# Performance work log

Measured on AMD Instinct MI355X. Metric: run time of the kernel, lower is better.

The kernel has to match this reference:

```python
import jax, jax.numpy as jnp
import numpy as np

EMB = 300
HID = 500
NUM_CLASSES = 20
WORD_VOCAB = 100000
ENT_VOCAB = 50
SEQ = 4096


def setup_inputs() -> dict:
    key = jax.random.key(0)
    ks = jax.random.split(key, 10)
    s = 0.05
    return {
        "ner_words": jax.random.randint(ks[0], (SEQ,), 0, WORD_VOCAB),
        "ner_labels": jax.random.randint(ks[1], (SEQ,), 0, ENT_VOCAB),
        "emb_word": jax.random.normal(ks[2], (WORD_VOCAB, EMB), jnp.float32) * s,
        "emb_ent": jax.random.normal(ks[3], (ENT_VOCAB, EMB), jnp.float32) * s,
        "W_ih": jax.random.normal(ks[4], (4 * HID, 2 * EMB), jnp.float32) * s,
        "W_hh": jax.random.normal(ks[5], (4 * HID, HID), jnp.float32) * s,
        "b_ih": jax.random.normal(ks[6], (4 * HID,), jnp.float32) * s,
        "b_hh": jax.random.normal(ks[7], (4 * HID,), jnp.float32) * s,
        "fc_w": jax.random.normal(ks[8], (NUM_CLASSES, HID), jnp.float32) * s,
        "fc_b": jax.random.normal(ks[9], (NUM_CLASSES,), jnp.float32) * s,
    }


def _lstm_last(x, W_ih, W_hh, b_ih, b_hh):
    # x: [N, 2*EMB]. PyTorch LSTM gate order: i, f, g, o.
    pre = x @ W_ih.T + (b_ih + b_hh)  # [N, 4H] input contribution precomputed

    def step(carry, p):
        h, c = carry
        gates = p + h @ W_hh.T  # [4H]
        i, f, g, o = jnp.split(gates, 4)
        i = jax.nn.sigmoid(i)
        f = jax.nn.sigmoid(f)
        g = jnp.tanh(g)
        o = jax.nn.sigmoid(o)
        c = f * c + i * g
        h = o * jnp.tanh(c)
        return (h, c), None

    h0 = jnp.zeros((HID,), x.dtype)
    c0 = jnp.zeros((HID,), x.dtype)
    (h, _), _ = jax.lax.scan(step, (h0, c0), pre)
    return h  # last hidden state == last LSTM output


def reference(ner_words, ner_labels, emb_word, emb_ent, W_ih, W_hh, b_ih, b_hh, fc_w, fc_b):
    # per-token embedding gather + concat -> [N, 600]
    x = jnp.concatenate([emb_word[ner_words], emb_ent[ner_labels]], axis=-1)
    h_last = _lstm_last(x, W_ih, W_hh, b_ih, b_hh)
    out = h_last @ fc_w.T + fc_b
    return out.reshape(1, -1)
```

## Files before the change

### kernel.cpp

```cpp
#include <hip/hip_runtime.h>

typedef unsigned int uint;
typedef unsigned long long u64;
typedef _Float16 f16x2 __attribute__((ext_vector_type(2)));

#define SEQ 4096
#define EMB 300
#define HID 500
#define NG 2000
#define KX 600
#define KXP 608

#define BM 64
#define BN 64
#define BK 16

#define NWG 25
#define UPW 20
#define TPB 640

#define HPAIR 8
#define HHALF (250 * HPAIR)
#define HTOT  (2 * HHALF)

__global__ __launch_bounds__(256) void gather_x(const int* __restrict__ words,
                                                const int* __restrict__ labels,
                                                const float* __restrict__ embw,
                                                const float* __restrict__ embe,
                                                float* __restrict__ x) {
  int t = blockIdx.x;
  int w = words[t], l = labels[t];
  const float* rw = embw + (size_t)w * EMB;
  const float* re = embe + (size_t)l * EMB;
  float* xr = x + (size_t)t * KXP;
  for (int k = threadIdx.x; k < KXP; k += 256) {
    float v = 0.f;
    if (k < EMB) v = rw[k];
    else if (k < KX) v = re[k - EMB];
    xr[k] = v;
  }
}

__global__ __launch_bounds__(256) void gemm_pre(const float* __restrict__ x,
                                                const float* __restrict__ Wih,
                                                const float* __restrict__ bih,
                                                const float* __restrict__ bhh,
                                                float* __restrict__ pre) {
  __shared__ float As[BK][BM + 4];
  __shared__ float Bs[BK][BN + 4];
  const int m0 = blockIdx.x * BM;
  const int n0 = blockIdx.y * BN;
  const int tid = threadIdx.x;
  const int tx = tid & 15, ty = tid >> 4;
  const int lrow = tid >> 2;
  const int lc4 = (tid & 3) << 2;
  float acc[4][4] = {};

  for (int kk = 0; kk < KX; kk += BK) {
    float4 av = *(const float4*)(x + (size_t)(m0 + lrow) * KXP + kk + lc4);
    int brow = n0 + lrow; if (brow >= NG) brow = 0;
    float4 bv;
    if (kk + lc4 + 3 < KX) {
      bv = *(const float4*)(Wih + (size_t)brow * KX + kk + lc4);
    } else {
      float tmp[4];
#pragma unroll
      for (int j = 0; j < 4; ++j) {
        int k = kk + lc4 + j;
        tmp[j] = (k < KX) ? Wih[(size_t)brow * KX + k] : 0.f;
      }
      bv = make_float4(tmp[0], tmp[1], tmp[2], tmp[3]);
    }
    As[lc4 + 0][lrow] = av.x; As[lc4 + 1][lrow] = av.y;
    As[lc4 + 2][lrow] = av.z; As[lc4 + 3][lrow] = av.w;
    Bs[lc4 + 0][lrow] = bv.x; Bs[lc4 + 1][lrow] = bv.y;
    Bs[lc4 + 2][lrow] = bv.z; Bs[lc4 + 3][lrow] = bv.w;
    __syncthreads();
#pragma unroll
    for (int k = 0; k < BK; ++k) {
      float4 a = *(const float4*)&As[k][ty << 2];
      float4 b = *(const float4*)&Bs[k][tx << 2];
      acc[0][0] += a.x * b.x; acc[0][1] += a.x * b.y; acc[0][2] += a.x * b.z; acc[0][3] += a.x * b.w;
      acc[1][0] += a.y * b.x; acc[1][1] += a.y * b.y; acc[1][2] += a.y * b.z; acc[1][3] += a.y * b.w;
      acc[2][0] += a.z * b.x; acc[2][1] += a.z * b.y; acc[2][2] += a.z * b.z; acc[2][3] += a.z * b.w;
      acc[3][0] += a.w * b.x; acc[3][1] += a.w * b.y; acc[3][2] += a.w * b.z; acc[3][3] += a.w * b.w;
    }
    __syncthreads();
  }
#pragma unroll
  for (int i = 0; i < 4; ++i) {
    int m = m0 + (ty << 2) + i;
#pragma unroll
    for (int j = 0; j < 4; ++j) {
      int n = n0 + (tx << 2) + j;
      if (n < NG) pre[(size_t)m * NG + n] = acc[i][j] + bih[n] + bhh[n];
    }
  }
}

__global__ void init_sync(u64* hbuf) {
  for (int i = threadIdx.x; i < HTOT; i += 1024) hbuf[i] = 0ull;
}

__device__ __forceinline__ float sigm(float x) { return 1.f / (1.f + __expf(-x)); }
__device__ __forceinline__ float fast_tanh(float x) {
  x = fminf(fmaxf(x, -15.f), 15.f);
  float e = __expf(2.f * x);
  return (e - 1.f) / (e + 1.f);
}
__device__ __forceinline__ f16x2 as_f16x2(uint u) {
  union { uint i; f16x2 h; } c; c.i = u; return c.h;
}
__device__ __forceinline__ uint f2h16(float f) {
  union { _Float16 h; unsigned short u; } c; c.h = (_Float16)f; return (uint)c.u;
}
#if __has_builtin(__builtin_amdgcn_fdot2)
__device__ __forceinline__ float FDOT2(f16x2 a, f16x2 b, float c) {
  return __builtin_amdgcn_fdot2(a, b, c, false);
}
#else
__device__ __forceinline__ float FDOT2(f16x2 a, f16x2 b, float c) {
  return c + (float)a.x * (float)b.x + (float)a.y * (float)b.y;
}
#endif

#define TAGMASK 0x0000FFFF0000FFFFull

__global__ __launch_bounds__(TPB) void lstm_seq(const float* __restrict__ pre,
                                                const float* __restrict__ Whh,
                                                const float* __restrict__ fcw,
                                                const float* __restrict__ fcb,
                                                uint* hbuf,
                                                float* __restrict__ out) {
  __shared__ uint h2b[2][256];
  const int g = blockIdx.x;
  const int tid = threadIdx.x;
  const int unit = tid >> 5;
  const int gi = (tid >> 3) & 3;
  const int cc = tid & 7;
  const int owner = ((tid & 31) == 0);
  const int base = tid & 32;
  const int my_prerow = gi * HID + g * UPW + unit;
  const int my_unit = g * UPW + unit;
  const int my_slot = (my_unit >> 1) * (2 * HPAIR) + (my_unit & 1);

  for (int i = tid; i < 512; i += TPB) ((uint*)h2b)[i] = 0u;

  uint wreg[32];
  {
    size_t grow = (size_t)(gi * HID + g * UPW + unit) * HID;
#pragma unroll
    for (int q = 0; q < 8; ++q) {
#pragma unroll
      for (int j = 0; j < 4; ++j) {
        int word = q * 32 + cc * 4 + j;
        int c2 = word * 2;
        float v0 = (c2 < HID) ? Whh[grow + c2] : 0.f;
        float v1 = (c2 + 1 < HID) ? Whh[grow + c2 + 1] : 0.f;
        wreg[q * 4 + j] = f2h16(v0) | (f2h16(v1) << 16);
      }
    }
  }

  const u64* hb64 = (const u64*)hbuf;
  float c_reg = 0.f;

  for (int t = 0; t < SEQ; ++t) {
    float pre_v = 0.f;
    if (cc == 0) pre_v = pre[(size_t)t * NG + my_prerow];

    const u64 want2 = (u64)((uint)t & 0xffffu) * 0x0000000100000001ull;
    if (tid < 250) {
      const u64* src = hb64 + (size_t)(t & 1) * HHALF + (size_t)tid * HPAIR;
      u64 a = __hip_atomic_load(src, __ATOMIC_RELAXED, __HIP_MEMORY_SCOPE_AGENT);
      u64 b = __hip_atomic_load(src, __ATOMIC_RELAXED, __HIP_MEMORY_SCOPE_AGENT);
      for (;;) {
        if ((a & TAGMASK) == want2) break;
        if ((b & TAGMASK) == want2) { a = b; break; }
        a = __hip_atomic_load(src, __ATOMIC_RELAXED, __HIP_MEMORY_SCOPE_AGENT);
        b = __hip_atomic_load(src, __ATOMIC_RELAXED, __HIP_MEMORY_SCOPE_AGENT);
      }
      h2b[t & 1][tid] = (((uint)(a >> 16)) & 0xffffu) | (((uint)(a >> 48)) << 16);
    }
    __syncthreads();

    const uint* h2 = h2b[t & 1];
    float acc = 0.f;
#pragma unroll
    for (int q = 0; q < 8; ++q) {
      uint4 hh = *(const uint4*)&h2[q * 32 + cc * 4];
      acc = FDOT2(as_f16x2(wreg[q * 4 + 0]), as_f16x2(hh.x), acc);
      acc = FDOT2(as_f16x2(wreg[q * 4 + 1]), as_f16x2(hh.y), acc);
      acc = FDOT2(as_f16x2(wreg[q * 4 + 2]), as_f16x2(hh.z), acc);
      acc = FDOT2(as_f16x2(wreg[q * 4 + 3]), as_f16x2(hh.w), acc);
    }
    acc += __shfl_xor(acc, 1);
    acc += __shfl_xor(acc, 2);
    acc += __shfl_xor(acc, 4);
    if (cc == 0) acc += pre_v;

    float si = __shfl(acc, base + 0);
    float sf = __shfl(acc, base + 8);
    float sg = __shfl(acc, base + 16);
    float so = __shfl(acc, base + 24);
    if (owner) {
      float iv = sigm(si);
      float fv = sigm(sf);
      float gv = fast_tanh(sg);
      float ov = sigm(so);
      c_reg = fv * c_reg + iv * gv;
      float h = ov * fast_tanh(c_reg);
      uint pk = (f2h16(h) << 16) | ((uint)(t + 1) & 0xffffu);
      __hip_atomic_store(&hbuf[((t + 1) & 1) * (2 * HHALF) + my_slot], pk,
                         __ATOMIC_RELAXED, __HIP_MEMORY_SCOPE_AGENT);
    }
  }

  if (g == 0) {
    const u64 want2 = (u64)((uint)SEQ & 0xffffu) * 0x0000000100000001ull;
    if (tid < 250) {
      const u64* src = hb64 + (size_t)tid * HPAIR;
      u64 a;
      do {
        a = __hip_atomic_load(src, __ATOMIC_RELAXED, __HIP_MEMORY_SCOPE_AGENT);
      } while ((a & TAGMASK) != want2);
      h2b[0][tid] = (((uint)(a >> 16)) & 0xffffu) | (((uint)(a >> 48)) << 16);
    }
    __syncthreads();
    int row = tid >> 5, ln = tid & 31;
    float s = 0.f;
    for (int j = ln; j < HID; j += 32) {
      f16x2 p = as_f16x2(h2b[0][j >> 1]);
      float hv = (j & 1) ? (float)p.y : (float)p.x;
      s += fcw[row * HID + j] * hv;
    }
    s += __shfl_xor(s, 1); s += __shfl_xor(s, 2);
    s += __shfl_xor(s, 4); s += __shfl_xor(s, 8);
    s += __shfl_xor(s, 16);
    if (ln == 0) out[row] = s + fcb[row];
  }
}

extern "C" void kernel_launch(void* const* d_in, const int* in_sizes, int n_in,
                              void* d_out, int out_size, void* d_ws, size_t ws_size,
                              hipStream_t stream) {
  const int* words = (const int*)d_in[0];
  const int* labels = (const int*)d_in[1];
  const float* embw = (const float*)d_in[2];
  const float* embe = (const float*)d_in[3];
  const float* Wih = (const float*)d_in[4];
  const float* Whh = (const float*)d_in[5];
  const float* bih = (const float*)d_in[6];
  const float* bhh = (const float*)d_in[7];
  const float* fcw = (const float*)d_in[8];
  const float* fcb = (const float*)d_in[9];
  float* out = (float*)d_out;

  char* ws = (char*)d_ws;
  float* x = (float*)ws;
  float* pre = (float*)(ws + (size_t)SEQ * KXP * 4);
  uint* hbuf = (uint*)(ws + (size_t)SEQ * KXP * 4 + (size_t)SEQ * NG * 4);

  gather_x<<<SEQ, 256, 0, stream>>>(words, labels, embw, embe, x);
  dim3 ggrid(SEQ / BM, (NG + BN - 1) / BN);
  gemm_pre<<<ggrid, 256, 0, stream>>>(x, Wih, bih, bhh, pre);
  init_sync<<<1, 1024, 0, stream>>>((u64*)hbuf);
  lstm_seq<<<NWG, TPB, 0, stream>>>(pre, Whh, fcw, fcb, hbuf, out);
}
```

Baseline: 9.273 ms.

## Pin LSTM workgroups to a single XCC and poll via L2-coherent loads

The kernel now launches extra workgroups, and each reads its XCC id and takes a ticket. The first XCC to collect 25 workgroups becomes the active set, and all other workgroups exit. With every participant on one XCC, the per-step hidden-state exchange can poll with sc0 loads served by the shared L2 instead of agent-scope loads, falling back to agent-scope loads after repeated misses. Polling is spread over more threads, one pair each, and the next step's pre-activation is prefetched after the barrier. The risks are that correctness depends on workgroup co-residency and XCC placement, and that the inline asm and spin-wait startup add overhead.

```diff
diff --git a/kernel.cpp b/kernel.cpp
--- a/kernel.cpp
+++ b/kernel.cpp
@@ -18,6 +18,7 @@
 #define NWG 25
 #define UPW 20
 #define TPB 640
+#define NLAUNCH 256
 
 #define HPAIR 8
 #define HHALF (250 * HPAIR)
@@ -98,8 +99,9 @@
   }
 }
 
-__global__ void init_sync(u64* hbuf) {
+__global__ void init_sync(u64* hbuf, int* ctl) {
   for (int i = threadIdx.x; i < HTOT; i += 1024) hbuf[i] = 0ull;
+  if (threadIdx.x < 64) ctl[threadIdx.x] = (threadIdx.x == 0) ? -1 : 0;
 }
 
 __device__ __forceinline__ float sigm(float x) { return 1.f / (1.f + __expf(-x)); }
@@ -124,22 +126,71 @@
 }
 #endif
 
+__device__ __forceinline__ u64 ld_l2(const u64* p) {
+  u64 v;
+  asm volatile("global_load_dwordx2 %0, %1, off sc0\n\t"
+               "s_waitcnt vmcnt(0)"
+               : "=v"(v) : "v"(p) : "memory");
+  return v;
+}
+__device__ __forceinline__ u64 ld_agent(const u64* p) {
+  return __hip_atomic_load(p, __ATOMIC_RELAXED, __HIP_MEMORY_SCOPE_AGENT);
+}
+
 #define TAGMASK 0x0000FFFF0000FFFFull
+#define FASTCAP 16
+
+__device__ __forceinline__ u64 poll_pair(const u64* src, u64 want2) {
+  u64 a = ld_l2(src);
+  int miss = 0;
+  while ((a & TAGMASK) != want2) {
+    if (++miss >= FASTCAP) {
+      a = ld_agent(src);
+      if ((a & TAGMASK) == want2) break;
+    }
+    a = ld_l2(src);
+  }
+  return a;
+}
 
 __global__ __launch_bounds__(TPB) void lstm_seq(const float* __restrict__ pre,
                                                 const float* __restrict__ Whh,
                                                 const float* __restrict__ fcw,
                                                 const float* __restrict__ fcb,
-                                                uint* hbuf,
+                                                uint* hbuf, int* ctl,
                                                 float* __restrict__ out) {
-  __shared__ uint h2b[2][256];
-  const int g = blockIdx.x;
+  __shared__ __attribute__((aligned(16))) uint h2b[2][256];
+  __shared__ int s_slot;
   const int tid = threadIdx.x;
+
+  if (tid == 0) {
+    uint xcc;
+    asm volatile("s_getreg_b32 %0, hwreg(HW_REG_XCC_ID)" : "=s"(xcc));
+    xcc &= 7u;
+    int ticket = atomicAdd(&ctl[16 + (int)xcc], 1);
+    int slot = -1;
+    if (ticket < NWG) {
+      if (ticket == NWG - 1) atomicCAS(&ctl[0], -1, (int)xcc);
+      int w;
+      do {
+        __builtin_amdgcn_s_sleep(1);
+        w = __hip_atomic_load(&ctl[0], __ATOMIC_RELAXED, __HIP_MEMORY_SCOPE_AGENT);
+      } while (w == -1);
+      if (w == (int)xcc) slot = ticket;
+    }
+    s_slot = slot;
+  }
+  __syncthreads();
+  const int g = s_slot;
+  if (g < 0) return;
+
   const int unit = tid >> 5;
   const int gi = (tid >> 3) & 3;
   const int cc = tid & 7;
   const int owner = ((tid & 31) == 0);
   const int base = tid & 32;
+  const int poller = (tid & 1) && (tid < 500);
+  const int pidx = tid >> 1;
   const int my_prerow = gi * HID + g * UPW + unit;
   const int my_unit = g * UPW + unit;
   const int my_slot = (my_unit >> 1) * (2 * HPAIR) + (my_unit & 1);
@@ -165,24 +216,20 @@
   const u64* hb64 = (const u64*)hbuf;
   float c_reg = 0.f;
 
+  float pre_v = 0.f;
+  if (cc == 0) pre_v = pre[my_prerow];
+
   for (int t = 0; t < SEQ; ++t) {
-    float pre_v = 0.f;
-    if (cc == 0) pre_v = pre[(size_t)t * NG + my_prerow];
-
     const u64 want2 = (u64)((uint)t & 0xffffu) * 0x0000000100000001ull;
-    if (tid < 250) {
-      const u64* src = hb64 + (size_t)(t & 1) * HHALF + (size_t)tid * HPAIR;
-      u64 a = __hip_atomic_load(src, __ATOMIC_RELAXED, __HIP_MEMORY_SCOPE_AGENT);
-      u64 b = __hip_atomic_load(src, __ATOMIC_RELAXED, __HIP_MEMORY_SCOPE_AGENT);
-      for (;;) {
-        if ((a & TAGMASK) == want2) break;
-        if ((b & TAGMASK) == want2) { a = b; break; }
-        a = __hip_atomic_load(src, __ATOMIC_RELAXED, __HIP_MEMORY_SCOPE_AGENT);
-        b = __hip_atomic_load(src, __ATOMIC_RELAXED, __HIP_MEMORY_SCOPE_AGENT);
-      }
-      h2b[t & 1][tid] = (((uint)(a >> 16)) & 0xffffu) | (((uint)(a >> 48)) << 16);
+    if (poller) {
+      const u64* src = hb64 + (size_t)(t & 1) * HHALF + (size_t)pidx * HPAIR;
+      u64 a = poll_pair(src, want2);
+      h2b[t & 1][pidx] = (((uint)(a >> 16)) & 0xffffu) | (((uint)(a >> 48)) << 16);
     }
     __syncthreads();
+
+    float pre_nx = 0.f;
+    if (cc == 0 && t + 1 < SEQ) pre_nx = pre[(size_t)(t + 1) * NG + my_prerow];
 
     const uint* h2 = h2b[t & 1];
     float acc = 0.f;
@@ -214,17 +261,15 @@
       __hip_atomic_store(&hbuf[((t + 1) & 1) * (2 * HHALF) + my_slot], pk,
                          __ATOMIC_RELAXED, __HIP_MEMORY_SCOPE_AGENT);
     }
+    pre_v = pre_nx;
   }
 
   if (g == 0) {
     const u64 want2 = (u64)((uint)SEQ & 0xffffu) * 0x0000000100000001ull;
-    if (tid < 250) {
-      const u64* src = hb64 + (size_t)tid * HPAIR;
-      u64 a;
-      do {
-        a = __hip_atomic_load(src, __ATOMIC_RELAXED, __HIP_MEMORY_SCOPE_AGENT);
-      } while ((a & TAGMASK) != want2);
-      h2b[0][tid] = (((uint)(a >> 16)) & 0xffffu) | (((uint)(a >> 48)) << 16);
+    if (poller) {
+      const u64* src = hb64 + (size_t)pidx * HPAIR;
+      u64 a = poll_pair(src, want2);
+      h2b[0][pidx] = (((uint)(a >> 16)) & 0xffffu) | (((uint)(a >> 48)) << 16);
     }
     __syncthreads();
     int row = tid >> 5, ln = tid & 31;
@@ -257,13 +302,16 @@
   float* out = (float*)d_out;
 
   char* ws = (char*)d_ws;
+  const size_t X = (size_t)SEQ * KXP * 4;
+  const size_t P = (size_t)SEQ * NG * 4;
   float* x = (float*)ws;
-  float* pre = (float*)(ws + (size_t)SEQ * KXP * 4);
-  uint* hbuf = (uint*)(ws + (size_t)SEQ * KXP * 4 + (size_t)SEQ * NG * 4);
+  float* pre = (float*)(ws + X);
+  uint* hbuf = (uint*)(ws + X + P);
+  int* ctl = (int*)(ws + X + P + 32000);
 
   gather_x<<<SEQ, 256, 0, stream>>>(words, labels, embw, embe, x);
   dim3 ggrid(SEQ / BM, (NG + BN - 1) / BN);
   gemm_pre<<<ggrid, 256, 0, stream>>>(x, Wih, bih, bhh, pre);
-  init_sync<<<1, 1024, 0, stream>>>((u64*)hbuf);
-  lstm_seq<<<NWG, TPB, 0, stream>>>(pre, Whh, fcw, fcb, hbuf, out);
-}
+  init_sync<<<1, 1024, 0, stream>>>((u64*)hbuf, ctl);
+  lstm_seq<<<NLAUNCH, TPB, 0, stream>>>(pre, Whh, fcw, fcb, hbuf, ctl, out);
+}
```

Result: slower. 15.29 ms (+64.9%).

## Split LSTM block into dedicated polling waves and compute waves, prefetch next pre

Applied to the files above, without the earlier changes.

Adds 256 polling threads per block that spin on the tagged hidden-state buffer, while the 640 compute threads only run the dot products and gate math. The next step's pre-activation is prefetched one step ahead, so that load latency is off the critical path. Bounded spin guards are added to the polling loops. The extra waves raise block size to 896 threads, which could increase register pressure. The guards can break out early and read stale data if a step is slow.

```diff
diff --git a/kernel.cpp b/kernel.cpp
--- a/kernel.cpp
+++ b/kernel.cpp
@@ -17,7 +17,12 @@
 
 #define NWG 25
 #define UPW 20
-#define TPB 640
+#define NPOLL 256
+#define NCOMP 640
+#define TPB (NPOLL + NCOMP)
+
+#define STEP_GUARD 4096
+#define FC_GUARD   (1 << 20)
 
 #define HPAIR 8
 #define HHALF (250 * HPAIR)
@@ -124,6 +129,10 @@
 }
 #endif
 
+__device__ __forceinline__ u64 ld_agent(const u64* p) {
+  return __hip_atomic_load(p, __ATOMIC_RELAXED, __HIP_MEMORY_SCOPE_AGENT);
+}
+
 #define TAGMASK 0x0000FFFF0000FFFFull
 
 __global__ __launch_bounds__(TPB) void lstm_seq(const float* __restrict__ pre,
@@ -132,13 +141,15 @@
                                                 const float* __restrict__ fcb,
                                                 uint* hbuf,
                                                 float* __restrict__ out) {
-  __shared__ uint h2b[2][256];
+  __shared__ __attribute__((aligned(16))) uint h2b[2][256];
   const int g = blockIdx.x;
   const int tid = threadIdx.x;
-  const int unit = tid >> 5;
-  const int gi = (tid >> 3) & 3;
-  const int cc = tid & 7;
-  const int owner = ((tid & 31) == 0);
+  const bool pwave = tid < NPOLL;
+  const int local = pwave ? 0 : tid - NPOLL;
+  const int unit = local >> 5;
+  const int gi = (local >> 3) & 3;
+  const int cc = local & 7;
+  const int owner = !pwave && ((local & 31) == 0);
   const int base = tid & 32;
   const int my_prerow = gi * HID + g * UPW + unit;
   const int my_unit = g * UPW + unit;
@@ -147,7 +158,7 @@
   for (int i = tid; i < 512; i += TPB) ((uint*)h2b)[i] = 0u;
 
   uint wreg[32];
-  {
+  if (!pwave) {
     size_t grow = (size_t)(gi * HID + g * UPW + unit) * HID;
 #pragma unroll
     for (int q = 0; q < 8; ++q) {
@@ -165,79 +176,93 @@
   const u64* hb64 = (const u64*)hbuf;
   float c_reg = 0.f;
 
+  float pre_v = 0.f;
+  if (!pwave && cc == 0) pre_v = pre[my_prerow];
+
   for (int t = 0; t < SEQ; ++t) {
-    float pre_v = 0.f;
-    if (cc == 0) pre_v = pre[(size_t)t * NG + my_prerow];
-
-    const u64 want2 = (u64)((uint)t & 0xffffu) * 0x0000000100000001ull;
-    if (tid < 250) {
-      const u64* src = hb64 + (size_t)(t & 1) * HHALF + (size_t)tid * HPAIR;
-      u64 a = __hip_atomic_load(src, __ATOMIC_RELAXED, __HIP_MEMORY_SCOPE_AGENT);
-      u64 b = __hip_atomic_load(src, __ATOMIC_RELAXED, __HIP_MEMORY_SCOPE_AGENT);
-      for (;;) {
-        if ((a & TAGMASK) == want2) break;
-        if ((b & TAGMASK) == want2) { a = b; break; }
-        a = __hip_atomic_load(src, __ATOMIC_RELAXED, __HIP_MEMORY_SCOPE_AGENT);
-        b = __hip_atomic_load(src, __ATOMIC_RELAXED, __HIP_MEMORY_SCOPE_AGENT);
-      }
-      h2b[t & 1][tid] = (((uint)(a >> 16)) & 0xffffu) | (((uint)(a >> 48)) << 16);
-    }
-    __syncthreads();
-
-    const uint* h2 = h2b[t & 1];
-    float acc = 0.f;
-#pragma unroll
-    for (int q = 0; q < 8; ++q) {
-      uint4 hh = *(const uint4*)&h2[q * 32 + cc * 4];
-      acc = FDOT2(as_f16x2(wreg[q * 4 + 0]), as_f16x2(hh.x), acc);
-      acc = FDOT2(as_f16x2(wreg[q * 4 + 1]), as_f16x2(hh.y), acc);
-      acc = FDOT2(as_f16x2(wreg[q * 4 + 2]), as_f16x2(hh.z), acc);
-      acc = FDOT2(as_f16x2(wreg[q * 4 + 3]), as_f16x2(hh.w), acc);
-    }
-    acc += __shfl_xor(acc, 1);
-    acc += __shfl_xor(acc, 2);
-    acc += __shfl_xor(acc, 4);
-    if (cc == 0) acc += pre_v;
-
-    float si = __shfl(acc, base + 0);
-    float sf = __shfl(acc, base + 8);
-    float sg = __shfl(acc, base + 16);
-    float so = __shfl(acc, base + 24);
-    if (owner) {
-      float iv = sigm(si);
-      float fv = sigm(sf);
-      float gv = fast_tanh(sg);
-      float ov = sigm(so);
-      c_reg = fv * c_reg + iv * gv;
-      float h = ov * fast_tanh(c_reg);
-      uint pk = (f2h16(h) << 16) | ((uint)(t + 1) & 0xffffu);
-      __hip_atomic_store(&hbuf[((t + 1) & 1) * (2 * HHALF) + my_slot], pk,
-                         __ATOMIC_RELAXED, __HIP_MEMORY_SCOPE_AGENT);
+    if (pwave) {
+      if (tid < 250) {
+        const u64 want2 = (u64)((uint)t & 0xffffu) * 0x0000000100000001ull;
+        const u64* src = hb64 + (size_t)(t & 1) * HHALF + (size_t)tid * HPAIR;
+        u64 a = ld_agent(src);
+        u64 b = ld_agent(src);
+        int guard = 0;
+        for (;;) {
+          if ((a & TAGMASK) == want2) break;
+          if ((b & TAGMASK) == want2) { a = b; break; }
+          if (++guard > STEP_GUARD) break;
+          a = ld_agent(src);
+          b = ld_agent(src);
+        }
+        h2b[t & 1][tid] = (((uint)(a >> 16)) & 0xffffu) | (((uint)(a >> 48)) << 16);
+      }
+    }
+    __syncthreads();
+
+    if (!pwave) {
+      float pre_nx = 0.f;
+      if (cc == 0 && t + 1 < SEQ) pre_nx = pre[(size_t)(t + 1) * NG + my_prerow];
+
+      const uint* h2 = h2b[t & 1];
+      float acc = 0.f;
+#pragma unroll
+      for (int q = 0; q < 8; ++q) {
+        uint4 hh = *(const uint4*)&h2[q * 32 + cc * 4];
+        acc = FDOT2(as_f16x2(wreg[q * 4 + 0]), as_f16x2(hh.x), acc);
+        acc = FDOT2(as_f16x2(wreg[q * 4 + 1]), as_f16x2(hh.y), acc);
+        acc = FDOT2(as_f16x2(wreg[q * 4 + 2]), as_f16x2(hh.z), acc);
+        acc = FDOT2(as_f16x2(wreg[q * 4 + 3]), as_f16x2(hh.w), acc);
+      }
+      acc += __shfl_xor(acc, 1);
+      acc += __shfl_xor(acc, 2);
+      acc += __shfl_xor(acc, 4);
+      if (cc == 0) acc += pre_v;
+
+      float si = __shfl(acc, base + 0);
+      float sf = __shfl(acc, base + 8);
+      float sg = __shfl(acc, base + 16);
+      float so = __shfl(acc, base + 24);
+      if (owner) {
+        float iv = sigm(si);
+        float fv = sigm(sf);
+        float gv = fast_tanh(sg);
+        float ov = sigm(so);
+        c_reg = fv * c_reg + iv * gv;
+        float h = ov * fast_tanh(c_reg);
+        uint pk = (f2h16(h) << 16) | ((uint)(t + 1) & 0xffffu);
+        __hip_atomic_store(&hbuf[((t + 1) & 1) * (2 * HHALF) + my_slot], pk,
+                           __ATOMIC_RELAXED, __HIP_MEMORY_SCOPE_AGENT);
+      }
+      pre_v = pre_nx;
     }
   }
 
   if (g == 0) {
-    const u64 want2 = (u64)((uint)SEQ & 0xffffu) * 0x0000000100000001ull;
-    if (tid < 250) {
+    if (pwave && tid < 250) {
+      const u64 want2 = (u64)((uint)SEQ & 0xffffu) * 0x0000000100000001ull;
       const u64* src = hb64 + (size_t)tid * HPAIR;
-      u64 a;
-      do {
-        a = __hip_atomic_load(src, __ATOMIC_RELAXED, __HIP_MEMORY_SCOPE_AGENT);
-      } while ((a & TAGMASK) != want2);
+      u64 a = ld_agent(src);
+      int guard = 0;
+      while ((a & TAGMASK) != want2) {
+        if (++guard > FC_GUARD) break;
+        a = ld_agent(src);
+      }
       h2b[0][tid] = (((uint)(a >> 16)) & 0xffffu) | (((uint)(a >> 48)) << 16);
     }
     __syncthreads();
-    int row = tid >> 5, ln = tid & 31;
-    float s = 0.f;
-    for (int j = ln; j < HID; j += 32) {
-      f16x2 p = as_f16x2(h2b[0][j >> 1]);
-      float hv = (j & 1) ? (float)p.y : (float)p.x;
-      s += fcw[row * HID + j] * hv;
-    }
-    s += __shfl_xor(s, 1); s += __shfl_xor(s, 2);
-    s += __shfl_xor(s, 4); s += __shfl_xor(s, 8);
-    s += __shfl_xor(s, 16);
-    if (ln == 0) out[row] = s + fcb[row];
+    if (!pwave) {
+      int row = local >> 5, ln = local & 31;
+      float s = 0.f;
+      for (int j = ln; j < HID; j += 32) {
+        f16x2 p = as_f16x2(h2b[0][j >> 1]);
+        float hv = (j & 1) ? (float)p.y : (float)p.x;
+        s += fcw[row * HID + j] * hv;
+      }
+      s += __shfl_xor(s, 1); s += __shfl_xor(s, 2);
+      s += __shfl_xor(s, 4); s += __shfl_xor(s, 8);
+      s += __shfl_xor(s, 16);
+      if (ln == 0) out[row] = s + fcb[row];
+    }
   }
 }
 
@@ -257,9 +282,11 @@
   float* out = (float*)d_out;
 
   char* ws = (char*)d_ws;
+  const size_t X = (size_t)SEQ * KXP * 4;
+  const size_t P = (size_t)SEQ * NG * 4;
   float* x = (float*)ws;
-  float* pre = (float*)(ws + (size_t)SEQ * KXP * 4);
-  uint* hbuf = (uint*)(ws + (size_t)SEQ * KXP * 4 + (size_t)SEQ * NG * 4);
+  float* pre = (float*)(ws + X);
+  uint* hbuf = (uint*)(ws + X + P);
 
   gather_x<<<SEQ, 256, 0, stream>>>(words, labels, embw, embe, x);
   dim3 ggrid(SEQ / BM, (NG + BN - 1) / BN);
```

After: 11.67 ms. 25.8% more time.
